# Optimization experiments

Hardware: AMD Instinct MI355X
Metric: run time of the kernel (lower is better)

The kernel has to match this reference:

```python
import jax, jax.numpy as jnp
import numpy as np

B, S, D, H = 8, 1024, 256, 8
HD = D // H
EPS = 1e-5
NEG = -1000000000.0


def setup_inputs() -> dict:
    key = jax.random.key(0)
    ks = jax.random.split(key, 12)
    s = 1.0 / np.sqrt(D)
    inp = {
        "q": jax.random.normal(ks[0], (B, S, D), jnp.float32),
        "kv_mask": jax.random.randint(ks[1], (B, S), 0, 2) > 0,
        "attn_bias": jax.random.normal(ks[2], (B, S, S, H), jnp.float32),
        "Wq": jax.random.normal(ks[3], (D, D), jnp.float32) * s,
        "bq": jax.random.normal(ks[4], (D,), jnp.float32) * s,
        "Wk": jax.random.normal(ks[5], (D, D), jnp.float32) * s,
        "bk": jax.random.normal(ks[6], (D,), jnp.float32) * s,
        "Wv": jax.random.normal(ks[7], (D, D), jnp.float32) * s,
        "bv": jax.random.normal(ks[8], (D,), jnp.float32) * s,
        "gamma": jnp.ones((D,), jnp.float32),
        "beta": jnp.zeros((D,), jnp.float32),
        "Wo": jax.random.normal(ks[9], (D, D), jnp.float32) * s,
        "bo": jax.random.normal(ks[10], (D,), jnp.float32) * s,
    }
    return inp


def reference(q, kv_mask, attn_bias, Wq, bq, Wk, bk, Wv, bv, gamma, beta, Wo, bo):
    b, s, d = q.shape
    # merge_masks: q_mask all True -> merged = kv_mask broadcast over query dim
    merged = jnp.broadcast_to(kv_mask[:, None, None, :], (b, 1, s, s))  # [b,1,s,s]
    # additive float mask: (~mask)*-1e9 + bias permuted to [b,h,q,k]
    add_mask = (~merged).astype(q.dtype) * NEG + jnp.transpose(attn_bias, (0, 3, 1, 2))
    # projections (torch Linear: x @ W.T + b)
    qh = (q @ Wq.T + bq).reshape(b, s, H, HD).transpose(0, 2, 1, 3)  # [b,h,s,hd]
    kh = (q @ Wk.T + bk).reshape(b, s, H, HD).transpose(0, 2, 1, 3)
    vh = (q @ Wv.T + bv).reshape(b, s, H, HD).transpose(0, 2, 1, 3)
    scores = jnp.einsum("bhqd,bhkd->bhqk", qh, kh) / np.sqrt(HD) + add_mask
    attn = jax.nn.softmax(scores, axis=-1)
    a = jnp.einsum("bhqk,bhkd->bhqd", attn, vh)  # [b,h,s,hd]
    a = a.transpose(0, 2, 1, 3).reshape(b, s, d)
    # LayerNorm (eps=1e-5)
    mu = a.mean(-1, keepdims=True)
    var = ((a - mu) ** 2).mean(-1, keepdims=True)
    a = (a - mu) / jnp.sqrt(var + EPS) * gamma + beta
    return a @ Wo.T + bo
```

## Files before the change

### kernel.cpp

```cpp
#include <hip/hip_runtime.h>
#include <hip/hip_bf16.h>


static constexpr int SEQ = 1024;
static constexpr float SCL  = 0.17677669529663687f;
static constexpr float NEGV = -1000000000.0f;

typedef __attribute__((ext_vector_type(8))) __bf16 bf8v;
typedef __attribute__((ext_vector_type(4))) float  f4v;

__device__ __forceinline__ f4v mfma16(bf8v a, bf8v b, f4v c) {
  return __builtin_amdgcn_mfma_f32_16x16x32_bf16(a, b, c, 0, 0, 0);
}
__device__ __forceinline__ unsigned short bfbits(float f) {
  __hip_bfloat16 hbf = __float2bfloat16(f);
  unsigned short u; __builtin_memcpy(&u, &hbf, 2); return u;
}

__global__ __launch_bounds__(256) void prep_kernel(
    const float* __restrict__ q, const float* __restrict__ Wq,
    const float* __restrict__ Wk, const float* __restrict__ Wv,
    const float* __restrict__ Wo, const int* __restrict__ km,
    __hip_bfloat16* __restrict__ q_bf, __hip_bfloat16* __restrict__ w_bf,
    float* __restrict__ mskf)
{
  const int NQ4 = (8192 * 256) / 4;
  const int NW4 = 65536 / 4;
  int t = threadIdx.x;

  if (blockIdx.x == 2304) {
    __shared__ int isbool;
    if (t == 0) isbool = 0;
    __syncthreads();
    const unsigned* u = (const unsigned*)km;
    int any = 0;
    for (int i = t; i < 2048; i += 256)
      if (u[i] & ~1u) any = 1;
    if (any) isbool = 1;
    __syncthreads();
    const unsigned char* b8 = (const unsigned char*)km;
    for (int i = t; i < 8192; i += 256) {
      int mv = isbool ? (int)b8[i] : km[i];
      mskf[i] = mv ? 0.f : NEGV;
    }
    return;
  }

  int i = blockIdx.x * 256 + t;
  const float4* src; __hip_bfloat16* dst;
  if (i < NQ4) {
    src = (const float4*)q + i;
    dst = q_bf + (long)i * 4;
  } else {
    int j = i - NQ4; int w = j >> 14; int o4 = j & (NW4 - 1);
    const float* sp = (w == 0) ? Wq : (w == 1) ? Wk : (w == 2) ? Wv : Wo;
    src = (const float4*)sp + o4;
    dst = w_bf + w * 65536 + o4 * 4;
  }
  float4 v = *src;
  ushort4 pk;
  pk.x = bfbits(v.x); pk.y = bfbits(v.y); pk.z = bfbits(v.z); pk.w = bfbits(v.w);
  *reinterpret_cast<ushort4*>(dst) = pk;
}

__global__ __launch_bounds__(256) void qkv_gemm(
    const __hip_bfloat16* __restrict__ q_bf, const __hip_bfloat16* __restrict__ w_bf,
    const float* __restrict__ bq, const float* __restrict__ bk,
    const float* __restrict__ bv,
    __hip_bfloat16* __restrict__ qh, __hip_bfloat16* __restrict__ kh,
    __hip_bfloat16* __restrict__ vt)
{
  int z = blockIdx.z;
  int w = threadIdx.x >> 6;
  int l = threadIdx.x & 63, lr = l & 15, lg = l >> 4;

  const __hip_bfloat16 *A, *Bm; const float* bias; __hip_bfloat16* out;
  long ldOut; int m0, n0;
  if (z < 2) {
    A = q_bf; Bm = w_bf + z * 65536; bias = z ? bk : bq; out = z ? kh : qh;
    ldOut = 256;
    m0 = blockIdx.x * 64; n0 = blockIdx.y * 128 + w * 32;
  } else {
    A = w_bf + 2 * 65536; Bm = q_bf; bias = bv; out = vt; ldOut = 8192;
    int bid = blockIdx.y * 128 + blockIdx.x;
    m0 = (bid >> 6) * 64; n0 = (bid & 63) * 128 + w * 32;
  }

  f4v acc[4][2];
#pragma unroll
  for (int mt = 0; mt < 4; ++mt)
#pragma unroll
    for (int nt = 0; nt < 2; ++nt) acc[mt][nt] = f4v{0.f, 0.f, 0.f, 0.f};

  const __hip_bfloat16* Ab = A  + (long)(m0 + lr) * 256 + lg * 8;
  const __hip_bfloat16* Bb = Bm + (long)(n0 + lr) * 256 + lg * 8;
#pragma unroll
  for (int k0 = 0; k0 < 256; k0 += 32) {
    bf8v af[4], bfr[2];
#pragma unroll
    for (int mt = 0; mt < 4; ++mt)
      af[mt] = *reinterpret_cast<const bf8v*>(Ab + (long)mt * 16 * 256 + k0);
#pragma unroll
    for (int nt = 0; nt < 2; ++nt)
      bfr[nt] = *reinterpret_cast<const bf8v*>(Bb + (long)nt * 16 * 256 + k0);
#pragma unroll
    for (int mt = 0; mt < 4; ++mt)
#pragma unroll
      for (int nt = 0; nt < 2; ++nt)
        acc[mt][nt] = mfma16(af[mt], bfr[nt], acc[mt][nt]);
  }

#pragma unroll
  for (int mt = 0; mt < 4; ++mt) {
    int mrow = m0 + mt * 16 + lg * 4;
#pragma unroll
    for (int nt = 0; nt < 2; ++nt) {
      int ncol = n0 + nt * 16 + lr;
#pragma unroll
      for (int r = 0; r < 4; ++r) {
        float v = acc[mt][nt][r] + ((z == 2) ? bias[mrow + r] : bias[ncol]);
        out[(long)(mrow + r) * ldOut + ncol] = __float2bfloat16(v);
      }
    }
  }
}

__global__ __launch_bounds__(512) void attn_kernel(
    const __hip_bfloat16* __restrict__ qh, const __hip_bfloat16* __restrict__ kh,
    const __hip_bfloat16* __restrict__ vt, const float* __restrict__ bias,
    const float* __restrict__ mskf, const __hip_bfloat16* __restrict__ wob,
    const float* __restrict__ gamma, const float* __restrict__ beta,
    const float* __restrict__ bo, float* __restrict__ outp)
{
  __shared__ __align__(16) char smem[48512];
  float* bsm = (float*)smem;
  float* msk = (float*)(smem + 34176);
  __hip_bfloat16* psm = (__hip_bfloat16*)(smem + 38272);
  float* osm = (float*)smem;
  __hip_bfloat16* ansm = (__hip_bfloat16*)(smem + 16704);

  int bb = blockIdx.x >> 6;
  int qt = blockIdx.x & 63;
  int h  = threadIdx.x >> 6;
  int l  = threadIdx.x & 63, lr = l & 15, lg = l >> 4;
  int q0 = qt * 16;
  long bS = (long)bb * SEQ;
  int t = threadIdx.x;

  for (int i = t; i < 1024; i += 512) msk[i] = mskf[bS + i];

  bf8v qf = *reinterpret_cast<const bf8v*>(qh + (bS + q0 + lr) * 256 + h * 32 + lg * 8);

  f4v o[2];
  o[0] = f4v{0.f, 0.f, 0.f, 0.f}; o[1] = f4v{0.f, 0.f, 0.f, 0.f};
  float mrun = -1e30f, lrun = 0.f;

  const float* bgbase = bias + (bS + q0) * 8192L;
  int qq0 = t >> 6;
  int c4  = t & 63;

  auto loadBias = [&](int kbase, float4 (&br)[2]) {
#pragma unroll
    for (int r2 = 0; r2 < 2; ++r2)
      br[r2] = *reinterpret_cast<const float4*>(
          bgbase + (long)(r2 * 8 + qq0) * 8192 + kbase * 8 + c4 * 4);
  };
  auto writeBias = [&](int buf, const float4 (&br)[2]) {
    float* bp = bsm + buf * (16 * 267);
    int kk = c4 >> 1, h0 = (c4 & 1) * 4;
#pragma unroll
    for (int r2 = 0; r2 < 2; ++r2) {
      int qq = r2 * 8 + qq0;
      float vv[4] = {br[r2].x, br[r2].y, br[r2].z, br[r2].w};
#pragma unroll
      for (int ii = 0; ii < 4; ++ii)
        bp[qq * 267 + (h0 + ii) * 33 + kk] = vv[ii];
    }
  };
  auto issueKV = [&](int kbase, bf8v (&kf)[2], bf8v (&vf)[2]) {
#pragma unroll
    for (int nt = 0; nt < 2; ++nt)
      kf[nt] = *reinterpret_cast<const bf8v*>(
          kh + (bS + kbase + nt * 16 + lr) * 256 + h * 32 + lg * 8);
#pragma unroll
    for (int n2 = 0; n2 < 2; ++n2)
      vf[n2] = *reinterpret_cast<const bf8v*>(
          vt + (long)(h * 32 + n2 * 16 + lr) * 8192 + bS + kbase + lg * 8);
  };

  float4 brA[2], brB[2];
  bf8v kfA[2], kfB[2], vfA[2], vfB[2];

  auto body = [&](int kt, float4 (&brN)[2],
                  bf8v (&kfC)[2], bf8v (&kfN)[2],
                  bf8v (&vfC)[2], bf8v (&vfN)[2]) {
    int kbase = kt * 32;
    bool more = (kt + 1 < 32);
    if (more) { loadBias(kbase + 32, brN); issueKV(kbase + 32, kfN, vfN); }

    const float* bp = bsm + (kt & 1) * (16 * 267) + lr * 267 + h * 33;

    f4v zero = f4v{0.f, 0.f, 0.f, 0.f};
    f4v s0 = mfma16(kfC[0], qf, zero);
    f4v s1 = mfma16(kfC[1], qf, zero);

    float v[8];
#pragma unroll
    for (int j = 0; j < 4; ++j) {
      int k0i = lg * 4 + j;
      v[j]     = s0[j] * SCL + bp[k0i]      + msk[kbase + k0i];
      v[4 + j] = s1[j] * SCL + bp[16 + k0i] + msk[kbase + 16 + k0i];
    }
    float tm = fmaxf(fmaxf(fmaxf(v[0], v[1]), fmaxf(v[2], v[3])),
                     fmaxf(fmaxf(v[4], v[5]), fmaxf(v[6], v[7])));
    tm = fmaxf(tm, __shfl_xor(tm, 16));
    tm = fmaxf(tm, __shfl_xor(tm, 32));
    float mn = fmaxf(mrun, tm);
    float al = __expf(mrun - mn);
    mrun = mn;
    float p[8]; float ts = 0.f;
#pragma unroll
    for (int j = 0; j < 8; ++j) { p[j] = __expf(v[j] - mn); ts += p[j]; }
    ts += __shfl_xor(ts, 16);
    ts += __shfl_xor(ts, 32);
    lrun = lrun * al + ts;

    __hip_bfloat16* pp = psm + h * 640 + lr * 40;
#pragma unroll
    for (int j = 0; j < 4; ++j) {
      pp[lg * 4 + j]      = __float2bfloat16(p[j]);
      pp[16 + lg * 4 + j] = __float2bfloat16(p[4 + j]);
    }

#pragma unroll
    for (int r = 0; r < 4; ++r) {
      float alr = __shfl(al, lg * 4 + r);
      o[0][r] *= alr; o[1][r] *= alr;
    }

    bf8v pa = *reinterpret_cast<const bf8v*>(psm + h * 640 + lr * 40 + lg * 8);
    o[0] = mfma16(pa, vfC[0], o[0]);
    o[1] = mfma16(pa, vfC[1], o[1]);

    if (more) writeBias((kt + 1) & 1, brN);
    __syncthreads();
  };

  loadBias(0, brA); issueKV(0, kfA, vfA);
  writeBias(0, brA);
  __syncthreads();

  for (int kt2 = 0; kt2 < 16; ++kt2) {
    body(2 * kt2,     brB, kfA, kfB, vfA, vfB);
    body(2 * kt2 + 1, brA, kfB, kfA, vfB, vfA);
  }

  float rinv = 1.f / lrun;
#pragma unroll
  for (int r = 0; r < 4; ++r) {
    float invr = __shfl(rinv, lg * 4 + r);
    int qq = lg * 4 + r;
    osm[qq * 261 + h * 32 + lr]      = o[0][r] * invr;
    osm[qq * 261 + h * 32 + 16 + lr] = o[1][r] * invr;
  }
  __syncthreads();

  {
    int row = t >> 5;
    int c8 = (t & 31) * 8;
    float vv[8]; float sm = 0.f, sq = 0.f;
#pragma unroll
    for (int j = 0; j < 8; ++j) {
      vv[j] = osm[row * 261 + c8 + j];
      sm += vv[j]; sq += vv[j] * vv[j];
    }
#pragma unroll
    for (int mm = 1; mm < 32; mm <<= 1) { sm += __shfl_xor(sm, mm); sq += __shfl_xor(sq, mm); }
    float mean = sm * (1.f / 256.f);
    float var  = sq * (1.f / 256.f) - mean * mean;
    float rstd = rsqrtf(var + 1e-5f);
    float4 g0 = *reinterpret_cast<const float4*>(gamma + c8);
    float4 g1 = *reinterpret_cast<const float4*>(gamma + c8 + 4);
    float4 b0 = *reinterpret_cast<const float4*>(beta + c8);
    float4 b1 = *reinterpret_cast<const float4*>(beta + c8 + 4);
    float gg[8] = {g0.x, g0.y, g0.z, g0.w, g1.x, g1.y, g1.z, g1.w};
    float bb8[8] = {b0.x, b0.y, b0.z, b0.w, b1.x, b1.y, b1.z, b1.w};
    ushort4 pkA, pkB;
    pkA.x = bfbits((vv[0] - mean) * rstd * gg[0] + bb8[0]);
    pkA.y = bfbits((vv[1] - mean) * rstd * gg[1] + bb8[1]);
    pkA.z = bfbits((vv[2] - mean) * rstd * gg[2] + bb8[2]);
    pkA.w = bfbits((vv[3] - mean) * rstd * gg[3] + bb8[3]);
    pkB.x = bfbits((vv[4] - mean) * rstd * gg[4] + bb8[4]);
    pkB.y = bfbits((vv[5] - mean) * rstd * gg[5] + bb8[5]);
    pkB.z = bfbits((vv[6] - mean) * rstd * gg[6] + bb8[6]);
    pkB.w = bfbits((vv[7] - mean) * rstd * gg[7] + bb8[7]);
    *reinterpret_cast<ushort4*>(&ansm[row * 264 + c8])     = pkA;
    *reinterpret_cast<ushort4*>(&ansm[row * 264 + c8 + 4]) = pkB;
  }
  __syncthreads();

  f4v acc2[2];
  acc2[0] = f4v{0.f, 0.f, 0.f, 0.f}; acc2[1] = f4v{0.f, 0.f, 0.f, 0.f};
#pragma unroll
  for (int k0 = 0; k0 < 256; k0 += 32) {
    bf8v afr = *reinterpret_cast<const bf8v*>(&ansm[lr * 264 + lg * 8 + k0]);
#pragma unroll
    for (int nt = 0; nt < 2; ++nt) {
      bf8v bfrg = *reinterpret_cast<const bf8v*>(
          wob + (long)(h * 32 + nt * 16 + lr) * 256 + lg * 8 + k0);
      acc2[nt] = mfma16(afr, bfrg, acc2[nt]);
    }
  }
#pragma unroll
  for (int nt = 0; nt < 2; ++nt) {
    int ocol = h * 32 + nt * 16 + lr;
    float bov = bo[ocol];
#pragma unroll
    for (int r = 0; r < 4; ++r) {
      int orow = q0 + lg * 4 + r;
      outp[(bS + orow) * 256 + ocol] = acc2[nt][r] + bov;
    }
  }
}

extern "C" void kernel_launch(void* const* d_in, const int* in_sizes, int n_in,
                              void* d_out, int out_size, void* d_ws, size_t ws_size,
                              hipStream_t stream) {
  const float* q   = (const float*)d_in[0];
  const int*   km  = (const int*)d_in[1];
  const float* bias = (const float*)d_in[2];
  const float* Wq = (const float*)d_in[3];
  const float* bq = (const float*)d_in[4];
  const float* Wk = (const float*)d_in[5];
  const float* bk = (const float*)d_in[6];
  const float* Wv = (const float*)d_in[7];
  const float* bv = (const float*)d_in[8];
  const float* gamma = (const float*)d_in[9];
  const float* beta  = (const float*)d_in[10];
  const float* Wo = (const float*)d_in[11];
  const float* bo = (const float*)d_in[12];

  char* wsb = (char*)d_ws;
  __hip_bfloat16* q_bf = (__hip_bfloat16*)(wsb + 0);
  __hip_bfloat16* qh   = (__hip_bfloat16*)(wsb + (4  << 20));
  __hip_bfloat16* kh   = (__hip_bfloat16*)(wsb + (8  << 20));
  __hip_bfloat16* vt   = (__hip_bfloat16*)(wsb + (12 << 20));
  __hip_bfloat16* wbf  = (__hip_bfloat16*)(wsb + (16 << 20));
  float*          mskf = (float*)         (wsb + (17 << 20));
  __hip_bfloat16* wob  = wbf + 196608;

  prep_kernel<<<2305, 256, 0, stream>>>(q, Wq, Wk, Wv, Wo, km, q_bf, wbf, mskf);
  qkv_gemm<<<dim3(128, 2, 3), 256, 0, stream>>>(q_bf, wbf, bq, bk, bv, qh, kh, vt);
  attn_kernel<<<512, 512, 0, stream>>>(qh, kh, vt, bias, mskf, wob,
                                       gamma, beta, bo, (float*)d_out);
}
```

Baseline: 138.7 us.

## Widen attention key tile to 64, stage bias+mask as bf16, fold scale into Q

```diff
diff --git a/kernel.cpp b/kernel.cpp
--- a/kernel.cpp
+++ b/kernel.cpp
@@ -15,6 +15,9 @@
 __device__ __forceinline__ unsigned short bfbits(float f) {
   __hip_bfloat16 hbf = __float2bfloat16(f);
   unsigned short u; __builtin_memcpy(&u, &hbf, 2); return u;
+}
+__device__ __forceinline__ float bf2f(unsigned short u) {
+  unsigned x = ((unsigned)u) << 16; float f; __builtin_memcpy(&f, &x, 4); return f;
 }
 
 __global__ __launch_bounds__(256) void prep_kernel(
@@ -119,23 +122,24 @@
 #pragma unroll
       for (int r = 0; r < 4; ++r) {
         float v = acc[mt][nt][r] + ((z == 2) ? bias[mrow + r] : bias[ncol]);
+        if (z == 0) v *= SCL;
         out[(long)(mrow + r) * ldOut + ncol] = __float2bfloat16(v);
       }
     }
   }
 }
 
-__global__ __launch_bounds__(512) void attn_kernel(
+__global__ __launch_bounds__(512, 4) void attn_kernel(
     const __hip_bfloat16* __restrict__ qh, const __hip_bfloat16* __restrict__ kh,
     const __hip_bfloat16* __restrict__ vt, const float* __restrict__ bias,
     const float* __restrict__ mskf, const __hip_bfloat16* __restrict__ wob,
     const float* __restrict__ gamma, const float* __restrict__ beta,
     const float* __restrict__ bo, float* __restrict__ outp)
 {
-  __shared__ __align__(16) char smem[48512];
-  float* bsm = (float*)smem;
-  float* msk = (float*)(smem + 34176);
-  __hip_bfloat16* psm = (__hip_bfloat16*)(smem + 38272);
+  __shared__ __align__(16) char smem[57600];
+  __hip_bfloat16* bsm = (__hip_bfloat16*)smem;
+  __hip_bfloat16* psm = (__hip_bfloat16*)(smem + 35072);
+  float* msk = (float*)(smem + 53504);
   float* osm = (float*)smem;
   __hip_bfloat16* ansm = (__hip_bfloat16*)(smem + 16704);
 
@@ -146,6 +150,7 @@
   int q0 = qt * 16;
   long bS = (long)bb * SEQ;
   int t = threadIdx.x;
+  int sq = t >> 5, skq = (t >> 1) & 15, shh = t & 1;
 
   for (int i = t; i < 1024; i += 512) msk[i] = mskf[bS + i];
 
@@ -155,81 +160,95 @@
   o[0] = f4v{0.f, 0.f, 0.f, 0.f}; o[1] = f4v{0.f, 0.f, 0.f, 0.f};
   float mrun = -1e30f, lrun = 0.f;
 
-  const float* bgbase = bias + (bS + q0) * 8192L;
-  int qq0 = t >> 6;
-  int c4  = t & 63;
-
-  auto loadBias = [&](int kbase, float4 (&br)[2]) {
-#pragma unroll
-    for (int r2 = 0; r2 < 2; ++r2)
-      br[r2] = *reinterpret_cast<const float4*>(
-          bgbase + (long)(r2 * 8 + qq0) * 8192 + kbase * 8 + c4 * 4);
+  const float* bgb = bias + (bS + q0 + sq) * 8192L + skq * 32 + shh * 4;
+
+  auto loadBias = [&](int kbase, float4 (&br)[4]) {
+#pragma unroll
+    for (int kk = 0; kk < 4; ++kk)
+      br[kk] = *reinterpret_cast<const float4*>(bgb + (long)kbase * 8 + kk * 8);
   };
-  auto writeBias = [&](int buf, const float4 (&br)[2]) {
-    float* bp = bsm + buf * (16 * 267);
-    int kk = c4 >> 1, h0 = (c4 & 1) * 4;
-#pragma unroll
-    for (int r2 = 0; r2 < 2; ++r2) {
-      int qq = r2 * 8 + qq0;
-      float vv[4] = {br[r2].x, br[r2].y, br[r2].z, br[r2].w};
-#pragma unroll
-      for (int ii = 0; ii < 4; ++ii)
-        bp[qq * 267 + (h0 + ii) * 33 + kk] = vv[ii];
+
+  auto cvtWrite = [&](int buf, const float4 (&br)[4], int kbase) {
+    float mk[4], w_[4][4];
+#pragma unroll
+    for (int kk = 0; kk < 4; ++kk) {
+      mk[kk] = msk[kbase + skq * 4 + kk];
+      w_[kk][0] = br[kk].x; w_[kk][1] = br[kk].y;
+      w_[kk][2] = br[kk].z; w_[kk][3] = br[kk].w;
+    }
+#pragma unroll
+    for (int ii = 0; ii < 4; ++ii) {
+      ushort4 hb;
+      hb.x = bfbits(w_[0][ii] + mk[0]);
+      hb.y = bfbits(w_[1][ii] + mk[1]);
+      hb.z = bfbits(w_[2][ii] + mk[2]);
+      hb.w = bfbits(w_[3][ii] + mk[3]);
+      *reinterpret_cast<ushort4*>(
+          bsm + buf * 8768 + sq * 548 + (shh * 4 + ii) * 68 + skq * 4) = hb;
     }
   };
-  auto issueKV = [&](int kbase, bf8v (&kf)[2], bf8v (&vf)[2]) {
-#pragma unroll
-    for (int nt = 0; nt < 2; ++nt)
-      kf[nt] = *reinterpret_cast<const bf8v*>(
-          kh + (bS + kbase + nt * 16 + lr) * 256 + h * 32 + lg * 8);
+
+  float4 brA[4], brB[4];
+  loadBias(0, brA);
+  loadBias(64, brB);
+  __syncthreads();
+  cvtWrite(0, brA, 0);
+  __syncthreads();
+
+  auto body = [&](int kt, float4 (&brIn)[4], float4 (&brHeld)[4]) {
+    int kbase = kt * 64;
+    if (kt + 2 < 16) loadBias(kbase + 128, brIn);
+
+    bf8v kf[4], vf[2][2];
+#pragma unroll
+    for (int u = 0; u < 4; ++u)
+      kf[u] = *reinterpret_cast<const bf8v*>(
+          kh + (bS + kbase + u * 16 + lr) * 256 + h * 32 + lg * 8);
 #pragma unroll
     for (int n2 = 0; n2 < 2; ++n2)
-      vf[n2] = *reinterpret_cast<const bf8v*>(
-          vt + (long)(h * 32 + n2 * 16 + lr) * 8192 + bS + kbase + lg * 8);
-  };
-
-  float4 brA[2], brB[2];
-  bf8v kfA[2], kfB[2], vfA[2], vfB[2];
-
-  auto body = [&](int kt, float4 (&brN)[2],
-                  bf8v (&kfC)[2], bf8v (&kfN)[2],
-                  bf8v (&vfC)[2], bf8v (&vfN)[2]) {
-    int kbase = kt * 32;
-    bool more = (kt + 1 < 32);
-    if (more) { loadBias(kbase + 32, brN); issueKV(kbase + 32, kfN, vfN); }
-
-    const float* bp = bsm + (kt & 1) * (16 * 267) + lr * 267 + h * 33;
-
-    f4v zero = f4v{0.f, 0.f, 0.f, 0.f};
-    f4v s0 = mfma16(kfC[0], qf, zero);
-    f4v s1 = mfma16(kfC[1], qf, zero);
-
-    float v[8];
-#pragma unroll
-    for (int j = 0; j < 4; ++j) {
-      int k0i = lg * 4 + j;
-      v[j]     = s0[j] * SCL + bp[k0i]      + msk[kbase + k0i];
-      v[4 + j] = s1[j] * SCL + bp[16 + k0i] + msk[kbase + 16 + k0i];
-    }
-    float tm = fmaxf(fmaxf(fmaxf(v[0], v[1]), fmaxf(v[2], v[3])),
-                     fmaxf(fmaxf(v[4], v[5]), fmaxf(v[6], v[7])));
+#pragma unroll
+      for (int s2 = 0; s2 < 2; ++s2)
+        vf[n2][s2] = *reinterpret_cast<const bf8v*>(
+            vt + (long)(h * 32 + n2 * 16 + lr) * 8192 + bS + kbase + s2 * 32 + lg * 8);
+
+    f4v z4 = f4v{0.f, 0.f, 0.f, 0.f};
+    f4v s[4];
+#pragma unroll
+    for (int u = 0; u < 4; ++u) s[u] = mfma16(kf[u], qf, z4);
+
+    const __hip_bfloat16* bp = bsm + (kt & 1) * 8768 + lr * 548 + h * 68;
+    float v[16];
+#pragma unroll
+    for (int u = 0; u < 4; ++u) {
+      ushort4 b4 = *reinterpret_cast<const ushort4*>(bp + u * 16 + lg * 4);
+      v[u * 4 + 0] = s[u][0] + bf2f(b4.x);
+      v[u * 4 + 1] = s[u][1] + bf2f(b4.y);
+      v[u * 4 + 2] = s[u][2] + bf2f(b4.z);
+      v[u * 4 + 3] = s[u][3] + bf2f(b4.w);
+    }
+
+    float tm = v[0];
+#pragma unroll
+    for (int i = 1; i < 16; ++i) tm = fmaxf(tm, v[i]);
     tm = fmaxf(tm, __shfl_xor(tm, 16));
     tm = fmaxf(tm, __shfl_xor(tm, 32));
     float mn = fmaxf(mrun, tm);
     float al = __expf(mrun - mn);
     mrun = mn;
-    float p[8]; float ts = 0.f;
-#pragma unroll
-    for (int j = 0; j < 8; ++j) { p[j] = __expf(v[j] - mn); ts += p[j]; }
+    float ts = 0.f, p[16];
+#pragma unroll
+    for (int i = 0; i < 16; ++i) { p[i] = __expf(v[i] - mn); ts += p[i]; }
     ts += __shfl_xor(ts, 16);
     ts += __shfl_xor(ts, 32);
     lrun = lrun * al + ts;
 
-    __hip_bfloat16* pp = psm + h * 640 + lr * 40;
-#pragma unroll
-    for (int j = 0; j < 4; ++j) {
-      pp[lg * 4 + j]      = __float2bfloat16(p[j]);
-      pp[16 + lg * 4 + j] = __float2bfloat16(p[4 + j]);
+    __hip_bfloat16* pw = psm + h * 1152 + lr * 72 + lg * 4;
+#pragma unroll
+    for (int u = 0; u < 4; ++u) {
+      ushort4 pk;
+      pk.x = bfbits(p[u * 4 + 0]); pk.y = bfbits(p[u * 4 + 1]);
+      pk.z = bfbits(p[u * 4 + 2]); pk.w = bfbits(p[u * 4 + 3]);
+      *reinterpret_cast<ushort4*>(pw + u * 16) = pk;
     }
 
 #pragma unroll
@@ -238,21 +257,20 @@
       o[0][r] *= alr; o[1][r] *= alr;
     }
 
-    bf8v pa = *reinterpret_cast<const bf8v*>(psm + h * 640 + lr * 40 + lg * 8);
-    o[0] = mfma16(pa, vfC[0], o[0]);
-    o[1] = mfma16(pa, vfC[1], o[1]);
-
-    if (more) writeBias((kt + 1) & 1, brN);
+#pragma unroll
+    for (int s2 = 0; s2 < 2; ++s2) {
+      bf8v pa = *reinterpret_cast<const bf8v*>(psm + h * 1152 + lr * 72 + s2 * 32 + lg * 8);
+      o[0] = mfma16(pa, vf[0][s2], o[0]);
+      o[1] = mfma16(pa, vf[1][s2], o[1]);
+    }
+
+    if (kt + 1 < 16) cvtWrite((kt + 1) & 1, brHeld, kbase + 64);
     __syncthreads();
   };
 
-  loadBias(0, brA); issueKV(0, kfA, vfA);
-  writeBias(0, brA);
-  __syncthreads();
-
-  for (int kt2 = 0; kt2 < 16; ++kt2) {
-    body(2 * kt2,     brB, kfA, kfB, vfA, vfB);
-    body(2 * kt2 + 1, brA, kfB, kfA, vfB, vfA);
+  for (int m = 0; m < 8; ++m) {
+    body(2 * m,     brA, brB);
+    body(2 * m + 1, brB, brA);
   }
 
   float rinv = 1.f / lrun;
@@ -268,16 +286,16 @@
   {
     int row = t >> 5;
     int c8 = (t & 31) * 8;
-    float vv[8]; float sm = 0.f, sq = 0.f;
+    float vv[8]; float sm = 0.f, sq2 = 0.f;
 #pragma unroll
     for (int j = 0; j < 8; ++j) {
       vv[j] = osm[row * 261 + c8 + j];
-      sm += vv[j]; sq += vv[j] * vv[j];
-    }
-#pragma unroll
-    for (int mm = 1; mm < 32; mm <<= 1) { sm += __shfl_xor(sm, mm); sq += __shfl_xor(sq, mm); }
+      sm += vv[j]; sq2 += vv[j] * vv[j];
+    }
+#pragma unroll
+    for (int mm = 1; mm < 32; mm <<= 1) { sm += __shfl_xor(sm, mm); sq2 += __shfl_xor(sq2, mm); }
     float mean = sm * (1.f / 256.f);
-    float var  = sq * (1.f / 256.f) - mean * mean;
+    float var  = sq2 * (1.f / 256.f) - mean * mean;
     float rstd = rsqrtf(var + 1e-5f);
     float4 g0 = *reinterpret_cast<const float4*>(gamma + c8);
     float4 g1 = *reinterpret_cast<const float4*>(gamma + c8 + 4);
```

Measured after the change: 148.0 us. 6.7% more time.

## Stage bias+mask as bf16 in LDS, fold scale into Q, reorder blocks

Applied to the files above, without the earlier changes.

```diff
diff --git a/kernel.cpp b/kernel.cpp
--- a/kernel.cpp
+++ b/kernel.cpp
@@ -15,6 +15,9 @@
 __device__ __forceinline__ unsigned short bfbits(float f) {
   __hip_bfloat16 hbf = __float2bfloat16(f);
   unsigned short u; __builtin_memcpy(&u, &hbf, 2); return u;
+}
+__device__ __forceinline__ float bf2f(unsigned short u) {
+  unsigned x = ((unsigned)u) << 16; float f; __builtin_memcpy(&f, &x, 4); return f;
 }
 
 __global__ __launch_bounds__(256) void prep_kernel(
@@ -119,33 +122,35 @@
 #pragma unroll
       for (int r = 0; r < 4; ++r) {
         float v = acc[mt][nt][r] + ((z == 2) ? bias[mrow + r] : bias[ncol]);
+        if (z == 0) v *= SCL;
         out[(long)(mrow + r) * ldOut + ncol] = __float2bfloat16(v);
       }
     }
   }
 }
 
-__global__ __launch_bounds__(512) void attn_kernel(
+__global__ __launch_bounds__(512, 4) void attn_kernel(
     const __hip_bfloat16* __restrict__ qh, const __hip_bfloat16* __restrict__ kh,
     const __hip_bfloat16* __restrict__ vt, const float* __restrict__ bias,
     const float* __restrict__ mskf, const __hip_bfloat16* __restrict__ wob,
     const float* __restrict__ gamma, const float* __restrict__ beta,
     const float* __restrict__ bo, float* __restrict__ outp)
 {
-  __shared__ __align__(16) char smem[48512];
-  float* bsm = (float*)smem;
-  float* msk = (float*)(smem + 34176);
-  __hip_bfloat16* psm = (__hip_bfloat16*)(smem + 38272);
+  __shared__ __align__(16) char smem[33024];
+  __hip_bfloat16* bsm = (__hip_bfloat16*)smem;
+  __hip_bfloat16* psm = (__hip_bfloat16*)(smem + 18688);
+  float* msk = (float*)(smem + 28928);
   float* osm = (float*)smem;
   __hip_bfloat16* ansm = (__hip_bfloat16*)(smem + 16704);
 
-  int bb = blockIdx.x >> 6;
-  int qt = blockIdx.x & 63;
+  int bb = blockIdx.x & 7;
+  int qt = blockIdx.x >> 3;
   int h  = threadIdx.x >> 6;
   int l  = threadIdx.x & 63, lr = l & 15, lg = l >> 4;
   int q0 = qt * 16;
   long bS = (long)bb * SEQ;
   int t = threadIdx.x;
+  int sq = t >> 5, kp = (t >> 2) & 7, hh = t & 3;
 
   for (int i = t; i < 1024; i += 512) msk[i] = mskf[bS + i];
 
@@ -155,62 +160,54 @@
   o[0] = f4v{0.f, 0.f, 0.f, 0.f}; o[1] = f4v{0.f, 0.f, 0.f, 0.f};
   float mrun = -1e30f, lrun = 0.f;
 
-  const float* bgbase = bias + (bS + q0) * 8192L;
-  int qq0 = t >> 6;
-  int c4  = t & 63;
-
-  auto loadBias = [&](int kbase, float4 (&br)[2]) {
-#pragma unroll
-    for (int r2 = 0; r2 < 2; ++r2)
-      br[r2] = *reinterpret_cast<const float4*>(
-          bgbase + (long)(r2 * 8 + qq0) * 8192 + kbase * 8 + c4 * 4);
+  const float* bgb = bias + (bS + q0 + sq) * 8192L + 2 * hh;
+
+  auto loadBias = [&](int tile, float2 (&br)[4]) {
+    int kb = tile * 32;
+#pragma unroll
+    for (int kk = 0; kk < 4; ++kk)
+      br[kk] = *reinterpret_cast<const float2*>(bgb + (long)(kb + 4 * kp + kk) * 8);
   };
-  auto writeBias = [&](int buf, const float4 (&br)[2]) {
-    float* bp = bsm + buf * (16 * 267);
-    int kk = c4 >> 1, h0 = (c4 & 1) * 4;
-#pragma unroll
-    for (int r2 = 0; r2 < 2; ++r2) {
-      int qq = r2 * 8 + qq0;
-      float vv[4] = {br[r2].x, br[r2].y, br[r2].z, br[r2].w};
-#pragma unroll
-      for (int ii = 0; ii < 4; ++ii)
-        bp[qq * 267 + (h0 + ii) * 33 + kk] = vv[ii];
-    }
+  auto cvtWrite = [&](int buf, const float2 (&br)[4], int tile) {
+    int kb = tile * 32;
+    float mk[4];
+#pragma unroll
+    for (int kk = 0; kk < 4; ++kk) mk[kk] = msk[kb + 4 * kp + kk];
+    __hip_bfloat16* bp = bsm + buf * 4672 + sq * 292 + 4 * kp;
+    ushort4 h0, h1;
+    h0.x = bfbits(br[0].x + mk[0]); h0.y = bfbits(br[1].x + mk[1]);
+    h0.z = bfbits(br[2].x + mk[2]); h0.w = bfbits(br[3].x + mk[3]);
+    h1.x = bfbits(br[0].y + mk[0]); h1.y = bfbits(br[1].y + mk[1]);
+    h1.z = bfbits(br[2].y + mk[2]); h1.w = bfbits(br[3].y + mk[3]);
+    *reinterpret_cast<ushort4*>(bp + (2 * hh) * 36)     = h0;
+    *reinterpret_cast<ushort4*>(bp + (2 * hh + 1) * 36) = h1;
   };
-  auto issueKV = [&](int kbase, bf8v (&kf)[2], bf8v (&vf)[2]) {
-#pragma unroll
-    for (int nt = 0; nt < 2; ++nt)
-      kf[nt] = *reinterpret_cast<const bf8v*>(
-          kh + (bS + kbase + nt * 16 + lr) * 256 + h * 32 + lg * 8);
-#pragma unroll
-    for (int n2 = 0; n2 < 2; ++n2)
-      vf[n2] = *reinterpret_cast<const bf8v*>(
-          vt + (long)(h * 32 + n2 * 16 + lr) * 8192 + bS + kbase + lg * 8);
-  };
-
-  float4 brA[2], brB[2];
-  bf8v kfA[2], kfB[2], vfA[2], vfB[2];
-
-  auto body = [&](int kt, float4 (&brN)[2],
-                  bf8v (&kfC)[2], bf8v (&kfN)[2],
-                  bf8v (&vfC)[2], bf8v (&vfN)[2]) {
+
+  auto compute = [&](int kt) {
     int kbase = kt * 32;
-    bool more = (kt + 1 < 32);
-    if (more) { loadBias(kbase + 32, brN); issueKV(kbase + 32, kfN, vfN); }
-
-    const float* bp = bsm + (kt & 1) * (16 * 267) + lr * 267 + h * 33;
-
-    f4v zero = f4v{0.f, 0.f, 0.f, 0.f};
-    f4v s0 = mfma16(kfC[0], qf, zero);
-    f4v s1 = mfma16(kfC[1], qf, zero);
+    bf8v kf0 = *reinterpret_cast<const bf8v*>(
+        kh + (bS + kbase + lr) * 256 + h * 32 + lg * 8);
+    bf8v kf1 = *reinterpret_cast<const bf8v*>(
+        kh + (bS + kbase + 16 + lr) * 256 + h * 32 + lg * 8);
+    bf8v vf0 = *reinterpret_cast<const bf8v*>(
+        vt + (long)(h * 32 + lr) * 8192 + bS + kbase + lg * 8);
+    bf8v vf1 = *reinterpret_cast<const bf8v*>(
+        vt + (long)(h * 32 + 16 + lr) * 8192 + bS + kbase + lg * 8);
+
+    f4v z4 = f4v{0.f, 0.f, 0.f, 0.f};
+    f4v s0 = mfma16(kf0, qf, z4);
+    f4v s1 = mfma16(kf1, qf, z4);
+
+    const __hip_bfloat16* bp = bsm + (kt & 1) * 4672 + lr * 292 + h * 36;
+    ushort4 b0 = *reinterpret_cast<const ushort4*>(bp + lg * 4);
+    ushort4 b1 = *reinterpret_cast<const ushort4*>(bp + 16 + lg * 4);
 
     float v[8];
-#pragma unroll
-    for (int j = 0; j < 4; ++j) {
-      int k0i = lg * 4 + j;
-      v[j]     = s0[j] * SCL + bp[k0i]      + msk[kbase + k0i];
-      v[4 + j] = s1[j] * SCL + bp[16 + k0i] + msk[kbase + 16 + k0i];
-    }
+    v[0] = s0[0] + bf2f(b0.x); v[1] = s0[1] + bf2f(b0.y);
+    v[2] = s0[2] + bf2f(b0.z); v[3] = s0[3] + bf2f(b0.w);
+    v[4] = s1[0] + bf2f(b1.x); v[5] = s1[1] + bf2f(b1.y);
+    v[6] = s1[2] + bf2f(b1.z); v[7] = s1[3] + bf2f(b1.w);
+
     float tm = fmaxf(fmaxf(fmaxf(v[0], v[1]), fmaxf(v[2], v[3])),
                      fmaxf(fmaxf(v[4], v[5]), fmaxf(v[6], v[7])));
     tm = fmaxf(tm, __shfl_xor(tm, 16));
@@ -225,12 +222,12 @@
     ts += __shfl_xor(ts, 32);
     lrun = lrun * al + ts;
 
-    __hip_bfloat16* pp = psm + h * 640 + lr * 40;
-#pragma unroll
-    for (int j = 0; j < 4; ++j) {
-      pp[lg * 4 + j]      = __float2bfloat16(p[j]);
-      pp[16 + lg * 4 + j] = __float2bfloat16(p[4 + j]);
-    }
+    __hip_bfloat16* pw = psm + h * 640 + lr * 40;
+    ushort4 p0, p1;
+    p0.x = bfbits(p[0]); p0.y = bfbits(p[1]); p0.z = bfbits(p[2]); p0.w = bfbits(p[3]);
+    p1.x = bfbits(p[4]); p1.y = bfbits(p[5]); p1.z = bfbits(p[6]); p1.w = bfbits(p[7]);
+    *reinterpret_cast<ushort4*>(pw + 4 * lg)      = p0;
+    *reinterpret_cast<ushort4*>(pw + 16 + 4 * lg) = p1;
 
 #pragma unroll
     for (int r = 0; r < 4; ++r) {
@@ -239,20 +236,28 @@
     }
 
     bf8v pa = *reinterpret_cast<const bf8v*>(psm + h * 640 + lr * 40 + lg * 8);
-    o[0] = mfma16(pa, vfC[0], o[0]);
-    o[1] = mfma16(pa, vfC[1], o[1]);
-
-    if (more) writeBias((kt + 1) & 1, brN);
-    __syncthreads();
+    o[0] = mfma16(pa, vf0, o[0]);
+    o[1] = mfma16(pa, vf1, o[1]);
   };
 
-  loadBias(0, brA); issueKV(0, kfA, vfA);
-  writeBias(0, brA);
+  float2 brA[4], brB[4];
+  loadBias(0, brA);
+  loadBias(1, brB);
   __syncthreads();
-
-  for (int kt2 = 0; kt2 < 16; ++kt2) {
-    body(2 * kt2,     brB, kfA, kfB, vfA, vfB);
-    body(2 * kt2 + 1, brA, kfB, kfA, vfB, vfA);
+  cvtWrite(0, brA, 0);
+  __syncthreads();
+
+  for (int m = 0; m < 16; ++m) {
+    { int kt = 2 * m;
+      if (kt + 2 < 32) loadBias(kt + 2, brA);
+      compute(kt);
+      cvtWrite(1, brB, kt + 1);
+      __syncthreads(); }
+    { int kt = 2 * m + 1;
+      if (kt + 2 < 32) loadBias(kt + 2, brB);
+      compute(kt);
+      if (kt < 31) cvtWrite(0, brA, kt + 1);
+      __syncthreads(); }
   }
 
   float rinv = 1.f / lrun;
@@ -268,16 +273,16 @@
   {
     int row = t >> 5;
     int c8 = (t & 31) * 8;
-    float vv[8]; float sm = 0.f, sq = 0.f;
+    float vv[8]; float sm = 0.f, sq2 = 0.f;
 #pragma unroll
     for (int j = 0; j < 8; ++j) {
       vv[j] = osm[row * 261 + c8 + j];
-      sm += vv[j]; sq += vv[j] * vv[j];
-    }
-#pragma unroll
-    for (int mm = 1; mm < 32; mm <<= 1) { sm += __shfl_xor(sm, mm); sq += __shfl_xor(sq, mm); }
+      sm += vv[j]; sq2 += vv[j] * vv[j];
+    }
+#pragma unroll
+    for (int mm = 1; mm < 32; mm <<= 1) { sm += __shfl_xor(sm, mm); sq2 += __shfl_xor(sq2, mm); }
     float mean = sm * (1.f / 256.f);
-    float var  = sq * (1.f / 256.f) - mean * mean;
+    float var  = sq2 * (1.f / 256.f) - mean * mean;
     float rstd = rsqrtf(var + 1e-5f);
     float4 g0 = *reinterpret_cast<const float4*>(gamma + c8);
     float4 g1 = *reinterpret_cast<const float4*>(gamma + c8 + 4);
```

After: 144.0 us. 1.04x slower.
